# Kernel tuning notes

Measured on AMD Instinct MI355X. Metric: run time of the kernel, lower is better.

## Reference

```python
import jax, jax.numpy as jnp
import numpy as np

IN_SIZES = [64, 128, 256]
HIDDEN = [512, 512]
ENC = 256
COUNTS = [100000, 80000, 60000]


def _xavier(key, fan_in, fan_out):
    # xavier_uniform with gain('sigmoid') == 1
    lim = float(np.sqrt(6.0 / (fan_in + fan_out)))
    return jax.random.uniform(key, (fan_in, fan_out), jnp.float32, -lim, lim)


def setup_inputs() -> dict:
    key = jax.random.key(0)
    ks = jax.random.split(key, 32)
    inp = {}
    ki = 0
    for t, (n, d) in enumerate(zip(COUNTS, IN_SIZES)):
        inp[f"x{t}"] = jax.random.normal(ks[ki], (n, d), dtype=jnp.float32)
        ki += 1
    # node_type sorted by type, counts match x tensors (invariant of the module)
    inp["node_type"] = jnp.concatenate(
        [jnp.full((n,), t, dtype=jnp.int32) for t, n in enumerate(COUNTS)])
    for t, d_in in enumerate(IN_SIZES):
        sizes = [d_in] + HIDDEN + [ENC]
        for i in range(len(sizes) - 1):
            inp[f"W{t}_{i+1}"] = _xavier(ks[ki], sizes[i], sizes[i + 1])
            ki += 1
            inp[f"b{t}_{i+1}"] = jnp.zeros((sizes[i + 1],), jnp.float32)
    return inp


def _mlp(x, layers):
    # each layer is Linear followed by Sigmoid (including the last)
    for W, b in layers:
        x = jax.nn.sigmoid(x @ W + b)
    return x


def reference(x0, x1, x2, node_type,
              W0_1, b0_1, W0_2, b0_2, W0_3, b0_3,
              W1_1, b1_1, W1_2, b1_2, W1_3, b1_3,
              W2_1, b2_1, W2_2, b2_2, W2_3, b2_3):
    xs = [x0, x1, x2]
    params = [
        [(W0_1, b0_1), (W0_2, b0_2), (W0_3, b0_3)],
        [(W1_1, b1_1), (W1_2, b1_2), (W1_3, b1_3)],
        [(W2_1, b2_1), (W2_2, b2_2), (W2_3, b2_3)],
    ]
    N = node_type.shape[0]
    X = jnp.zeros((N, ENC), dtype=jnp.float32)
    for nt in range(len(xs)):
        # static per-type count -> fixed-size nonzero works under jit
        idx = jnp.nonzero(node_type == nt, size=xs[nt].shape[0])[0]
        X = X.at[idx].set(_mlp(xs[nt], params[nt]))
    return X
```

## Files before the change

kernel.cpp:

```cpp
#include <hip/hip_runtime.h>
#include <hip/hip_bf16.h>

typedef __bf16 bf16x8 __attribute__((ext_vector_type(8)));
typedef __bf16 bf16x4 __attribute__((ext_vector_type(4)));
typedef float  f32x16 __attribute__((ext_vector_type(16)));

#define BM 128
#define S  520
#define SF 260
#define NT 4

struct PrepParams {
    const float* src[9];
    int Kt[9];
    int Mg[9];
    int N[9];
    int blkEnd[9];
    int unitBase[9];
};

__global__ void __launch_bounds__(256)
prep_weights(PrepParams p, uint4* __restrict__ dst) {
    __shared__ float tile[32][128];
    int b = blockIdx.x;
    int w = 0;
    while (b >= p.blkEnd[w]) ++w;
    int local = b - ((w == 0) ? 0 : p.blkEnd[w - 1]);
    int mgc = p.Mg[w];
    int kt = local / mgc;
    int mg = local - kt * mgc;
    const float* src = p.src[w];
    int N = p.N[w];
    int Kc = p.Kt[w] * 2;
    int t = threadIdx.x;

    int row0 = kt * 32, col0 = mg * 128;
#pragma unroll
    for (int i = 0; i < 4; ++i) {
        int e4 = t + i * 256;
        int r = e4 >> 5;
        int c4 = e4 & 31;
        float4 v = *(const float4*)&src[(size_t)(row0 + r) * N + col0 + c4 * 4];
        *(float4*)&tile[r][c4 * 4] = v;
    }
    __syncthreads();

#pragma unroll
    for (int rep = 0; rep < 2; ++rep) {
        int ul = t + rep * 256;
        int lane = ul & 63;
        int kcl = (ul >> 6) & 1;
        int mtl = ul >> 7;
        int gUnit = p.unitBase[w] +
                    ((mg * 4 + mtl) * Kc + (kt * 2 + kcl)) * 64 + lane;
        int lr = kcl * 16 + ((lane >> 5) << 3);
        int lc = mtl * 32 + (lane & 31);
        alignas(16) unsigned short u8[8];
#pragma unroll
        for (int j = 0; j < 8; ++j)
            u8[j] = __builtin_bit_cast(unsigned short, (__bf16)tile[lr + j][lc]);
        dst[gUnit] = *(const uint4*)u8;
    }
}

struct MlpParams {
    const float* X[3];
    const unsigned short* Wp[3];
    const float* B1[3];
    const float* B2[3];
    const float* B3[3];
    int dIn[3];
    int Nt[3];
    int rowOff[3];
    int blkStart[3];
};

__device__ __forceinline__ float sigmoidf(float z) {
    return __builtin_amdgcn_rcpf(
        1.0f + __builtin_amdgcn_exp2f(-1.442695040888963f * z));
}

template <int KC, int MT, bool TO_LDS>
__device__ __forceinline__ void layer(
    unsigned short* __restrict__ buf,
    const unsigned short* __restrict__ W,
    const float* __restrict__ bias,
    int wave, int lane)
{
    const int half = lane >> 5;
    const int lr = lane & 31;

    f32x16 acc[NT][MT];
#pragma unroll
    for (int n = 0; n < NT; ++n)
#pragma unroll
        for (int m = 0; m < MT; ++m)
#pragma unroll
            for (int e = 0; e < 16; ++e)
                acc[n][m][e] = 0.0f;

    const unsigned short* bp = buf + lr * S + half * 8;
    const unsigned short* ap = W + (size_t)wave * MT * KC * 512 + lane * 8;

    bf16x8 aPf[4][MT];
#pragma unroll
    for (int p = 0; p < 4; ++p)
#pragma unroll
        for (int m = 0; m < MT; ++m)
            aPf[p][m] = *(const bf16x8*)(ap + ((size_t)m * KC + p) * 512);

#pragma unroll
    for (int kc = 0; kc < KC; ++kc) {
        bf16x8 b[NT];
#pragma unroll
        for (int n = 0; n < NT; ++n)
            b[n] = *(const bf16x8*)(bp + (size_t)n * 32 * S + kc * 16);
#pragma unroll
        for (int m = 0; m < MT; ++m)
#pragma unroll
            for (int n = 0; n < NT; ++n)
                acc[n][m] = __builtin_amdgcn_mfma_f32_32x32x16_bf16(
                    aPf[kc & 3][m], b[n], acc[n][m], 0, 0, 0);
        if (kc + 4 < KC) {
#pragma unroll
            for (int m = 0; m < MT; ++m)
                aPf[kc & 3][m] =
                    *(const bf16x8*)(ap + ((size_t)m * KC + (kc + 4)) * 512);
        }
    }

    __syncthreads();

#pragma unroll
    for (int m = 0; m < MT; ++m) {
        int mt = wave * MT + m;
#pragma unroll
        for (int g = 0; g < 4; ++g) {
            int f0 = mt * 32 + g * 8 + half * 4;
            float4 bv = *(const float4*)(bias + f0);
#pragma unroll
            for (int n = 0; n < NT; ++n) {
                int r = n * 32 + lr;
                float s0 = sigmoidf(acc[n][m][g * 4 + 0] + bv.x);
                float s1 = sigmoidf(acc[n][m][g * 4 + 1] + bv.y);
                float s2 = sigmoidf(acc[n][m][g * 4 + 2] + bv.z);
                float s3 = sigmoidf(acc[n][m][g * 4 + 3] + bv.w);
                if constexpr (TO_LDS) {
                    bf16x4 h = {(__bf16)s0, (__bf16)s1, (__bf16)s2, (__bf16)s3};
                    *(bf16x4*)(buf + r * S + f0) = h;
                } else {
                    float* fb = (float*)buf;
                    *(float4*)(fb + r * SF + f0) =
                        make_float4(s0, s1, s2, s3);
                }
            }
        }
    }
}

__global__ void __launch_bounds__(512, 2)
mlp_fused(MlpParams p, float* __restrict__ out) {
    extern __shared__ unsigned short buf[];

    int nwg = gridDim.x;
    int bid = blockIdx.x;
    int q = nwg >> 3, r8 = nwg & 7;
    int xcd = bid & 7, lid = bid >> 3;
    int b = (xcd < r8 ? xcd * (q + 1) : r8 * (q + 1) + (xcd - r8) * q) + lid;

    int t = (b >= p.blkStart[1]) + (b >= p.blkStart[2]);
    int blk = b - p.blkStart[t];
    int dIn = p.dIn[t];
    int Nt = p.Nt[t];
    int row0 = blk * BM;
    const float* X = p.X[t];
    const unsigned short* W1 = p.Wp[t];
    const unsigned short* W2 = W1 + dIn * 512;
    const unsigned short* W3 = W2 + 512 * 512;

    int tid = threadIdx.x;
    int wave = tid >> 6;
    int lane = tid & 63;

    int d4 = dIn >> 2;
    int s4 = 31 - __clz(d4);
    int nf4 = BM * d4;
    for (int i = tid; i < nf4; i += 512) {
        int r = i >> s4;
        int c4 = i & (d4 - 1);
        int grow = row0 + r;
        float4 v = make_float4(0.f, 0.f, 0.f, 0.f);
        if (grow < Nt) v = ((const float4*)X)[(size_t)grow * d4 + c4];
        ushort4 u;
        u.x = __builtin_bit_cast(unsigned short, (__bf16)v.x);
        u.y = __builtin_bit_cast(unsigned short, (__bf16)v.y);
        u.z = __builtin_bit_cast(unsigned short, (__bf16)v.z);
        u.w = __builtin_bit_cast(unsigned short, (__bf16)v.w);
        *(ushort4*)(buf + r * S + c4 * 4) = u;
    }
    __syncthreads();

    if (t == 0)      layer< 4, 2, true>(buf, W1, p.B1[t], wave, lane);
    else if (t == 1) layer< 8, 2, true>(buf, W1, p.B1[t], wave, lane);
    else             layer<16, 2, true>(buf, W1, p.B1[t], wave, lane);
    __syncthreads();
    layer<32, 2, true>(buf, W2, p.B2[t], wave, lane);
    __syncthreads();
    layer<32, 1, false>(buf, W3, p.B3[t], wave, lane);
    __syncthreads();

    const float* fb = (const float*)buf;
    float* gOut = out + (size_t)(p.rowOff[t] + row0) * 256;
    for (int i = tid; i < BM * 64; i += 512) {
        int r = i >> 6;
        int c4 = i & 63;
        if (row0 + r < Nt)
            *(float4*)(gOut + r * 256 + c4 * 4) =
                *(const float4*)(fb + r * SF + c4 * 4);
    }
}

extern "C" void kernel_launch(void* const* d_in, const int* in_sizes, int n_in,
                              void* d_out, int out_size, void* d_ws, size_t ws_size,
                              hipStream_t stream) {
    const int IN0[3] = {64, 128, 256};
    const int CNT[3] = {100000, 80000, 60000};

    PrepParams pp;
    int blocks = 0, ubase = 0;
    for (int t = 0; t < 3; ++t) {
        int Ks[3] = {IN0[t], 512, 512};
        int Ns[3] = {512, 512, 256};
        for (int l = 0; l < 3; ++l) {
            int w = t * 3 + l;
            pp.src[w] = (const float*)d_in[4 + t * 6 + l * 2];
            pp.Kt[w] = Ks[l] >> 5;
            pp.Mg[w] = Ns[l] >> 7;
            pp.N[w] = Ns[l];
            pp.unitBase[w] = ubase;
            blocks += pp.Kt[w] * pp.Mg[w];
            pp.blkEnd[w] = blocks;
            ubase += (Ks[l] * Ns[l]) >> 3;
        }
    }
    prep_weights<<<dim3(blocks), dim3(256), 0, stream>>>(pp, (uint4*)d_ws);

    MlpParams mp;
    int woff = 0, roff = 0, boff = 0;
    for (int t = 0; t < 3; ++t) {
        mp.X[t] = (const float*)d_in[t];
        mp.Wp[t] = (const unsigned short*)d_ws + woff;
        mp.B1[t] = (const float*)d_in[4 + t * 6 + 1];
        mp.B2[t] = (const float*)d_in[4 + t * 6 + 3];
        mp.B3[t] = (const float*)d_in[4 + t * 6 + 5];
        mp.dIn[t] = IN0[t];
        mp.Nt[t] = CNT[t];
        mp.rowOff[t] = roff;
        mp.blkStart[t] = boff;
        woff += IN0[t] * 512 + 512 * 512 + 512 * 256;
        roff += CNT[t];
        boff += (CNT[t] + BM - 1) / BM;
    }
    size_t lds = (size_t)BM * S * sizeof(unsigned short);
    mlp_fused<<<dim3(boff), dim3(512), lds, stream>>>(mp, (float*)d_out);
}
```

Before: 657.9 us.

## Stream weights into LDS ring via async global-to-LDS loads with swizzled activations

Restructures the fused MLP kernel so each workgroup handles 64 rows with 4 waves. Weight tiles are no longer loaded per wave from global into registers; they are streamed into a double-buffered LDS ring with global_load_lds and consumed under explicit barriers and wait counts. The activation buffer uses an XOR swizzle in place of row padding, and the prepped weight layout is reordered to suit the new streaming order. This trades fewer rows per block, which means more weight traffic per output row, plus two barriers per k-step, for weight reuse shared across waves and loads that overlap the MFMAs.

```diff
diff --git a/kernel.cpp b/kernel.cpp
--- a/kernel.cpp
+++ b/kernel.cpp
@@ -5,10 +5,8 @@
 typedef __bf16 bf16x4 __attribute__((ext_vector_type(4)));
 typedef float  f32x16 __attribute__((ext_vector_type(16)));
 
-#define BM 128
-#define S  520
-#define SF 260
-#define NT 4
+#define MFMA __builtin_amdgcn_mfma_f32_32x32x16_bf16
+#define BM 64
 
 struct PrepParams {
     const float* src[9];
@@ -31,7 +29,6 @@
     int mg = local - kt * mgc;
     const float* src = p.src[w];
     int N = p.N[w];
-    int Kc = p.Kt[w] * 2;
     int t = threadIdx.x;
 
     int row0 = kt * 32, col0 = mg * 128;
@@ -51,8 +48,11 @@
         int lane = ul & 63;
         int kcl = (ul >> 6) & 1;
         int mtl = ul >> 7;
-        int gUnit = p.unitBase[w] +
-                    ((mg * 4 + mtl) * Kc + (kt * 2 + kcl)) * 64 + lane;
+        int mt = mg * 4 + mtl;
+        int k16 = kt * 2 + kcl;
+        int pidx = (N == 512) ? (k16 * 2 + (mt >> 3)) : k16;
+        int ml = mt & 7;
+        int gUnit = p.unitBase[w] + (pidx * 8 + ml) * 64 + lane;
         int lr = kcl * 16 + ((lane >> 5) << 3);
         int lc = mtl * 32 + (lane & 31);
         alignas(16) unsigned short u8[8];
@@ -80,87 +80,148 @@
         1.0f + __builtin_amdgcn_exp2f(-1.442695040888963f * z));
 }
 
-template <int KC, int MT, bool TO_LDS>
-__device__ __forceinline__ void layer(
-    unsigned short* __restrict__ buf,
-    const unsigned short* __restrict__ W,
-    const float* __restrict__ bias,
-    int wave, int lane)
+__device__ __forceinline__ unsigned swz(unsigned o) {
+    return o ^ (((o >> 10) & 31) << 4);
+}
+
+__device__ __forceinline__ void gload_lds16(const void* g, void* l) {
+    __builtin_amdgcn_global_load_lds(
+        (const __attribute__((address_space(1))) unsigned int*)g,
+        (__attribute__((address_space(3))) unsigned int*)l, 16, 0, 0);
+}
+
+__device__ __forceinline__ void halfstep(
+    const char* act, unsigned bo0, unsigned bo1, int k16,
+    const unsigned short* rc, unsigned short* rn,
+    const uint4*& wsrc, bool pf, int wave, int lane,
+    f32x16& a00, f32x16& a01, f32x16& a10, f32x16& a11)
 {
-    const int half = lane >> 5;
-    const int lr = lane & 31;
-
-    f32x16 acc[NT][MT];
-#pragma unroll
-    for (int n = 0; n < NT; ++n)
-#pragma unroll
-        for (int m = 0; m < MT; ++m)
-#pragma unroll
-            for (int e = 0; e < 16; ++e)
-                acc[n][m][e] = 0.0f;
-
-    const unsigned short* bp = buf + lr * S + half * 8;
-    const unsigned short* ap = W + (size_t)wave * MT * KC * 512 + lane * 8;
-
-    bf16x8 aPf[4][MT];
-#pragma unroll
-    for (int p = 0; p < 4; ++p)
-#pragma unroll
-        for (int m = 0; m < MT; ++m)
-            aPf[p][m] = *(const bf16x8*)(ap + ((size_t)m * KC + p) * 512);
-
-#pragma unroll
-    for (int kc = 0; kc < KC; ++kc) {
-        bf16x8 b[NT];
-#pragma unroll
-        for (int n = 0; n < NT; ++n)
-            b[n] = *(const bf16x8*)(bp + (size_t)n * 32 * S + kc * 16);
-#pragma unroll
-        for (int m = 0; m < MT; ++m)
-#pragma unroll
-            for (int n = 0; n < NT; ++n)
-                acc[n][m] = __builtin_amdgcn_mfma_f32_32x32x16_bf16(
-                    aPf[kc & 3][m], b[n], acc[n][m], 0, 0, 0);
-        if (kc + 4 < KC) {
-#pragma unroll
-            for (int m = 0; m < MT; ++m)
-                aPf[kc & 3][m] =
-                    *(const bf16x8*)(ap + ((size_t)m * KC + (kc + 4)) * 512);
+    unsigned o0 = bo0 + (unsigned)k16 * 32;
+    unsigned o1 = bo1 + (unsigned)k16 * 32;
+    bf16x8 b0 = *(const bf16x8*)(act + swz(o0));
+    bf16x8 b1 = *(const bf16x8*)(act + swz(o1));
+    if (pf) {
+        gload_lds16(wsrc + wave * 128 + lane,      rn + wave * 1024);
+        gload_lds16(wsrc + wave * 128 + 64 + lane, rn + wave * 1024 + 512);
+        wsrc += 512;
+        asm volatile("s_waitcnt vmcnt(2)" ::: "memory");
+    } else {
+        asm volatile("s_waitcnt vmcnt(0)" ::: "memory");
+    }
+    asm volatile("s_barrier" ::: "memory");
+    const unsigned short* ap = rc + wave * 1024 + lane * 8;
+    bf16x8 va0 = *(const bf16x8*)ap;
+    bf16x8 va1 = *(const bf16x8*)(ap + 512);
+    __builtin_amdgcn_s_setprio(1);
+    a00 = MFMA(va0, b0, a00, 0, 0, 0);
+    a10 = MFMA(va0, b1, a10, 0, 0, 0);
+    a01 = MFMA(va1, b0, a01, 0, 0, 0);
+    a11 = MFMA(va1, b1, a11, 0, 0, 0);
+    __builtin_amdgcn_s_setprio(0);
+    asm volatile("s_barrier" ::: "memory");
+}
+
+template <int K16>
+__device__ __forceinline__ void layer512(
+    char* act, unsigned short* ring, const uint4*& wsrc,
+    const float* bias, int wave, int lane, unsigned bo0, unsigned bo1)
+{
+    f32x16 acc[2][2][2];
+#pragma unroll
+    for (int h = 0; h < 2; ++h)
+#pragma unroll
+      for (int b = 0; b < 2; ++b)
+#pragma unroll
+        for (int m = 0; m < 2; ++m)
+#pragma unroll
+          for (int e = 0; e < 16; ++e) acc[h][b][m][e] = 0.f;
+
+#pragma unroll 2
+    for (int k16 = 0; k16 < K16; ++k16) {
+        halfstep(act, bo0, bo1, k16, ring,        ring + 4096, wsrc, true, wave, lane,
+                 acc[0][0][0], acc[0][0][1], acc[0][1][0], acc[0][1][1]);
+        halfstep(act, bo0, bo1, k16, ring + 4096, ring,        wsrc, true, wave, lane,
+                 acc[1][0][0], acc[1][0][1], acc[1][1][0], acc[1][1][1]);
+    }
+
+    int hv = lane >> 5, lr = lane & 31;
+#pragma unroll
+    for (int h = 0; h < 2; ++h)
+#pragma unroll
+      for (int m = 0; m < 2; ++m) {
+        int mt = h * 8 + wave * 2 + m;
+#pragma unroll
+        for (int g = 0; g < 4; ++g) {
+          int f0 = mt * 32 + g * 8 + hv * 4;
+          float4 bv = *(const float4*)(bias + f0);
+#pragma unroll
+          for (int bt = 0; bt < 2; ++bt) {
+            int r = bt * 32 + lr;
+            float s0 = sigmoidf(acc[h][bt][m][g * 4 + 0] + bv.x);
+            float s1 = sigmoidf(acc[h][bt][m][g * 4 + 1] + bv.y);
+            float s2 = sigmoidf(acc[h][bt][m][g * 4 + 2] + bv.z);
+            float s3 = sigmoidf(acc[h][bt][m][g * 4 + 3] + bv.w);
+            bf16x4 h4 = {(__bf16)s0, (__bf16)s1, (__bf16)s2, (__bf16)s3};
+            unsigned o = (unsigned)r * 1024 + (unsigned)f0 * 2;
+            *(bf16x4*)(act + swz(o)) = h4;
+          }
         }
-    }
-
-    __syncthreads();
-
-#pragma unroll
-    for (int m = 0; m < MT; ++m) {
-        int mt = wave * MT + m;
+      }
+    asm volatile("s_waitcnt lgkmcnt(0)" ::: "memory");
+    asm volatile("s_barrier" ::: "memory");
+}
+
+template <int K16>
+__device__ __forceinline__ void layer256(
+    char* act, unsigned short* ring, const uint4*& wsrc,
+    const float* bias, int wave, int lane, unsigned bo0, unsigned bo1)
+{
+    f32x16 acc[2][2];
+#pragma unroll
+    for (int b = 0; b < 2; ++b)
+#pragma unroll
+      for (int m = 0; m < 2; ++m)
+#pragma unroll
+        for (int e = 0; e < 16; ++e) acc[b][m][e] = 0.f;
+
+#pragma unroll 2
+    for (int kp = 0; kp < K16; kp += 2) {
+        halfstep(act, bo0, bo1, kp,     ring,        ring + 4096, wsrc, true,
+                 wave, lane, acc[0][0], acc[0][1], acc[1][0], acc[1][1]);
+        halfstep(act, bo0, bo1, kp + 1, ring + 4096, ring,        wsrc, (kp + 2 < K16),
+                 wave, lane, acc[0][0], acc[0][1], acc[1][0], acc[1][1]);
+    }
+
+    int hv = lane >> 5, lr = lane & 31;
+#pragma unroll
+    for (int m = 0; m < 2; ++m) {
+        int mt = wave * 2 + m;
 #pragma unroll
         for (int g = 0; g < 4; ++g) {
-            int f0 = mt * 32 + g * 8 + half * 4;
+            int f0 = mt * 32 + g * 8 + hv * 4;
             float4 bv = *(const float4*)(bias + f0);
 #pragma unroll
-            for (int n = 0; n < NT; ++n) {
-                int r = n * 32 + lr;
-                float s0 = sigmoidf(acc[n][m][g * 4 + 0] + bv.x);
-                float s1 = sigmoidf(acc[n][m][g * 4 + 1] + bv.y);
-                float s2 = sigmoidf(acc[n][m][g * 4 + 2] + bv.z);
-                float s3 = sigmoidf(acc[n][m][g * 4 + 3] + bv.w);
-                if constexpr (TO_LDS) {
-                    bf16x4 h = {(__bf16)s0, (__bf16)s1, (__bf16)s2, (__bf16)s3};
-                    *(bf16x4*)(buf + r * S + f0) = h;
-                } else {
-                    float* fb = (float*)buf;
-                    *(float4*)(fb + r * SF + f0) =
-                        make_float4(s0, s1, s2, s3);
-                }
+            for (int bt = 0; bt < 2; ++bt) {
+                int r = bt * 32 + lr;
+                float4 o4;
+                o4.x = sigmoidf(acc[bt][m][g * 4 + 0] + bv.x);
+                o4.y = sigmoidf(acc[bt][m][g * 4 + 1] + bv.y);
+                o4.z = sigmoidf(acc[bt][m][g * 4 + 2] + bv.z);
+                o4.w = sigmoidf(acc[bt][m][g * 4 + 3] + bv.w);
+                unsigned o = (unsigned)r * 1024 + (unsigned)f0 * 4;
+                *(float4*)(act + swz(o)) = o4;
             }
         }
     }
-}
-
-__global__ void __launch_bounds__(512, 2)
+    asm volatile("s_waitcnt lgkmcnt(0)" ::: "memory");
+    asm volatile("s_barrier" ::: "memory");
+}
+
+__global__ void __launch_bounds__(256, 2)
 mlp_fused(MlpParams p, float* __restrict__ out) {
-    extern __shared__ unsigned short buf[];
+    extern __shared__ char smem[];
+    char* act = smem;
+    unsigned short* ring = (unsigned short*)(smem + 65536);
 
     int nwg = gridDim.x;
     int bid = blockIdx.x;
@@ -174,18 +235,20 @@
     int Nt = p.Nt[t];
     int row0 = blk * BM;
     const float* X = p.X[t];
-    const unsigned short* W1 = p.Wp[t];
-    const unsigned short* W2 = W1 + dIn * 512;
-    const unsigned short* W3 = W2 + 512 * 512;
+    const uint4* wsrc = (const uint4*)p.Wp[t];
 
     int tid = threadIdx.x;
     int wave = tid >> 6;
     int lane = tid & 63;
 
+    gload_lds16(wsrc + wave * 128 + lane,      ring + wave * 1024);
+    gload_lds16(wsrc + wave * 128 + 64 + lane, ring + wave * 1024 + 512);
+    wsrc += 512;
+
     int d4 = dIn >> 2;
     int s4 = 31 - __clz(d4);
     int nf4 = BM * d4;
-    for (int i = tid; i < nf4; i += 512) {
+    for (int i = tid; i < nf4; i += 256) {
         int r = i >> s4;
         int c4 = i & (d4 - 1);
         int grow = row0 + r;
@@ -196,27 +259,28 @@
         u.y = __builtin_bit_cast(unsigned short, (__bf16)v.y);
         u.z = __builtin_bit_cast(unsigned short, (__bf16)v.z);
         u.w = __builtin_bit_cast(unsigned short, (__bf16)v.w);
-        *(ushort4*)(buf + r * S + c4 * 4) = u;
+        unsigned o = (unsigned)r * 1024 + (unsigned)c4 * 8;
+        *(ushort4*)(act + swz(o)) = u;
     }
     __syncthreads();
 
-    if (t == 0)      layer< 4, 2, true>(buf, W1, p.B1[t], wave, lane);
-    else if (t == 1) layer< 8, 2, true>(buf, W1, p.B1[t], wave, lane);
-    else             layer<16, 2, true>(buf, W1, p.B1[t], wave, lane);
-    __syncthreads();
-    layer<32, 2, true>(buf, W2, p.B2[t], wave, lane);
-    __syncthreads();
-    layer<32, 1, false>(buf, W3, p.B3[t], wave, lane);
-    __syncthreads();
-
-    const float* fb = (const float*)buf;
+    unsigned bo0 = (unsigned)(lane & 31) * 1024 + (unsigned)(lane >> 5) * 16;
+    unsigned bo1 = bo0 + 32 * 1024;
+
+    if (t == 0)      layer512<4 >(act, ring, wsrc, p.B1[0], wave, lane, bo0, bo1);
+    else if (t == 1) layer512<8 >(act, ring, wsrc, p.B1[1], wave, lane, bo0, bo1);
+    else             layer512<16>(act, ring, wsrc, p.B1[2], wave, lane, bo0, bo1);
+    layer512<32>(act, ring, wsrc, p.B2[t], wave, lane, bo0, bo1);
+    layer256<32>(act, ring, wsrc, p.B3[t], wave, lane, bo0, bo1);
+
     float* gOut = out + (size_t)(p.rowOff[t] + row0) * 256;
-    for (int i = tid; i < BM * 64; i += 512) {
+    for (int i = tid; i < BM * 64; i += 256) {
         int r = i >> 6;
         int c4 = i & 63;
-        if (row0 + r < Nt)
-            *(float4*)(gOut + r * 256 + c4 * 4) =
-                *(const float4*)(fb + r * SF + c4 * 4);
+        if (row0 + r < Nt) {
+            unsigned o = (unsigned)r * 1024 + (unsigned)c4 * 16;
+            *(float4*)(gOut + r * 256 + c4 * 4) = *(const float4*)(act + swz(o));
+        }
     }
 }
 
@@ -261,6 +325,6 @@
         roff += CNT[t];
         boff += (CNT[t] + BM - 1) / BM;
     }
-    size_t lds = (size_t)BM * S * sizeof(unsigned short);
-    mlp_fused<<<dim3(boff), dim3(512), lds, stream>>>(mp, (float*)d_out);
-}
+    size_t lds = 65536 + 2 * 8192;
+    mlp_fused<<<dim3(boff), dim3(256), lds, stream>>>(mp, (float*)d_out);
+}
```

New measurement: 707.8 us. 1.08x slower.

## Replace padded LDS activation layout with XOR swizzle and k-major weight packing

Applied to the files above, without the earlier changes.

The activation buffer changes from padded rows (stride 520 halves) to a dense 1024-byte row layout with an XOR swizzle, which cuts LDS use from about 133KB to 128KB and is meant to avoid bank conflicts. Packed weights are reordered k-major, so all m-tiles for one k-step sit next to each other, and the prefetch loop is restructured around that order. Barriers move inside the layer function. The risk is that the swizzle does not remove conflicts for the 16-byte B reads as well as padding did, and the different global access pattern for weights.

```diff
diff --git a/kernel.cpp b/kernel.cpp
--- a/kernel.cpp
+++ b/kernel.cpp
@@ -5,10 +5,8 @@
 typedef __bf16 bf16x4 __attribute__((ext_vector_type(4)));
 typedef float  f32x16 __attribute__((ext_vector_type(16)));
 
+#define MFMA __builtin_amdgcn_mfma_f32_32x32x16_bf16
 #define BM 128
-#define S  520
-#define SF 260
-#define NT 4
 
 struct PrepParams {
     const float* src[9];
@@ -31,7 +29,7 @@
     int mg = local - kt * mgc;
     const float* src = p.src[w];
     int N = p.N[w];
-    int Kc = p.Kt[w] * 2;
+    int NU = N >> 5;
     int t = threadIdx.x;
 
     int row0 = kt * 32, col0 = mg * 128;
@@ -51,8 +49,9 @@
         int lane = ul & 63;
         int kcl = (ul >> 6) & 1;
         int mtl = ul >> 7;
-        int gUnit = p.unitBase[w] +
-                    ((mg * 4 + mtl) * Kc + (kt * 2 + kcl)) * 64 + lane;
+        int mt = mg * 4 + mtl;
+        int k16 = kt * 2 + kcl;
+        int gUnit = p.unitBase[w] + (k16 * NU + mt) * 64 + lane;
         int lr = kcl * 16 + ((lane >> 5) << 3);
         int lc = mtl * 32 + (lane & 31);
         alignas(16) unsigned short u8[8];
@@ -80,53 +79,61 @@
         1.0f + __builtin_amdgcn_exp2f(-1.442695040888963f * z));
 }
 
-template <int KC, int MT, bool TO_LDS>
-__device__ __forceinline__ void layer(
-    unsigned short* __restrict__ buf,
-    const unsigned short* __restrict__ W,
+__device__ __forceinline__ unsigned swz(unsigned o) {
+    return o ^ (((o >> 10) & 31) << 4);
+}
+
+template <int K16, int NU, int MT, bool TO_LDS>
+__device__ __forceinline__ void layerR(
+    char* __restrict__ act,
+    const uint4* __restrict__ W,
     const float* __restrict__ bias,
     int wave, int lane)
 {
+    const int lr = lane & 31;
     const int half = lane >> 5;
-    const int lr = lane & 31;
-
-    f32x16 acc[NT][MT];
-#pragma unroll
-    for (int n = 0; n < NT; ++n)
+    const unsigned xm = (unsigned)lr << 4;
+    const unsigned bo = (unsigned)lr * 1024u + (unsigned)half * 16u;
+
+    f32x16 acc[MT][4];
+#pragma unroll
+    for (int m = 0; m < MT; ++m)
+#pragma unroll
+        for (int bt = 0; bt < 4; ++bt)
+#pragma unroll
+            for (int e = 0; e < 16; ++e) acc[m][bt][e] = 0.f;
+
+    const uint4* ap = W + (size_t)(wave * MT) * 64 + lane;
+
+    bf16x8 aPf[4][MT];
+#pragma unroll
+    for (int d = 0; d < 4; ++d)
 #pragma unroll
         for (int m = 0; m < MT; ++m)
-#pragma unroll
-            for (int e = 0; e < 16; ++e)
-                acc[n][m][e] = 0.0f;
-
-    const unsigned short* bp = buf + lr * S + half * 8;
-    const unsigned short* ap = W + (size_t)wave * MT * KC * 512 + lane * 8;
-
-    bf16x8 aPf[4][MT];
-#pragma unroll
-    for (int p = 0; p < 4; ++p)
+            aPf[d][m] = *(const bf16x8*)(ap + (size_t)(d * NU + m) * 64);
+
+#pragma unroll
+    for (int k = 0; k < K16; ++k) {
+        bf16x8 b[4];
+#pragma unroll
+        for (int bt = 0; bt < 4; ++bt) {
+            unsigned o = bo + (unsigned)bt * 32768u + (unsigned)k * 32u;
+            b[bt] = *(const bf16x8*)(act + (o ^ xm));
+        }
+        bf16x8 av[MT];
+#pragma unroll
+        for (int m = 0; m < MT; ++m) av[m] = aPf[k & 3][m];
+        if (k + 4 < K16) {
+#pragma unroll
+            for (int m = 0; m < MT; ++m)
+                aPf[k & 3][m] =
+                    *(const bf16x8*)(ap + (size_t)((k + 4) * NU + m) * 64);
+        }
 #pragma unroll
         for (int m = 0; m < MT; ++m)
-            aPf[p][m] = *(const bf16x8*)(ap + ((size_t)m * KC + p) * 512);
-
-#pragma unroll
-    for (int kc = 0; kc < KC; ++kc) {
-        bf16x8 b[NT];
-#pragma unroll
-        for (int n = 0; n < NT; ++n)
-            b[n] = *(const bf16x8*)(bp + (size_t)n * 32 * S + kc * 16);
-#pragma unroll
-        for (int m = 0; m < MT; ++m)
-#pragma unroll
-            for (int n = 0; n < NT; ++n)
-                acc[n][m] = __builtin_amdgcn_mfma_f32_32x32x16_bf16(
-                    aPf[kc & 3][m], b[n], acc[n][m], 0, 0, 0);
-        if (kc + 4 < KC) {
-#pragma unroll
-            for (int m = 0; m < MT; ++m)
-                aPf[kc & 3][m] =
-                    *(const bf16x8*)(ap + ((size_t)m * KC + (kc + 4)) * 512);
-        }
+#pragma unroll
+            for (int bt = 0; bt < 4; ++bt)
+                acc[m][bt] = MFMA(av[m], b[bt], acc[m][bt], 0, 0, 0);
     }
 
     __syncthreads();
@@ -139,28 +146,28 @@
             int f0 = mt * 32 + g * 8 + half * 4;
             float4 bv = *(const float4*)(bias + f0);
 #pragma unroll
-            for (int n = 0; n < NT; ++n) {
-                int r = n * 32 + lr;
-                float s0 = sigmoidf(acc[n][m][g * 4 + 0] + bv.x);
-                float s1 = sigmoidf(acc[n][m][g * 4 + 1] + bv.y);
-                float s2 = sigmoidf(acc[n][m][g * 4 + 2] + bv.z);
-                float s3 = sigmoidf(acc[n][m][g * 4 + 3] + bv.w);
+            for (int bt = 0; bt < 4; ++bt) {
+                int r = bt * 32 + lr;
+                float s0 = sigmoidf(acc[m][bt][g * 4 + 0] + bv.x);
+                float s1 = sigmoidf(acc[m][bt][g * 4 + 1] + bv.y);
+                float s2 = sigmoidf(acc[m][bt][g * 4 + 2] + bv.z);
+                float s3 = sigmoidf(acc[m][bt][g * 4 + 3] + bv.w);
                 if constexpr (TO_LDS) {
-                    bf16x4 h = {(__bf16)s0, (__bf16)s1, (__bf16)s2, (__bf16)s3};
-                    *(bf16x4*)(buf + r * S + f0) = h;
+                    bf16x4 h4 = {(__bf16)s0, (__bf16)s1, (__bf16)s2, (__bf16)s3};
+                    *(bf16x4*)(act + swz((unsigned)r * 1024u + (unsigned)f0 * 2u)) = h4;
                 } else {
-                    float* fb = (float*)buf;
-                    *(float4*)(fb + r * SF + f0) =
+                    *(float4*)(act + swz((unsigned)r * 1024u + (unsigned)f0 * 4u)) =
                         make_float4(s0, s1, s2, s3);
                 }
             }
         }
     }
+    __syncthreads();
 }
 
 __global__ void __launch_bounds__(512, 2)
 mlp_fused(MlpParams p, float* __restrict__ out) {
-    extern __shared__ unsigned short buf[];
+    extern __shared__ char act[];
 
     int nwg = gridDim.x;
     int bid = blockIdx.x;
@@ -174,9 +181,9 @@
     int Nt = p.Nt[t];
     int row0 = blk * BM;
     const float* X = p.X[t];
-    const unsigned short* W1 = p.Wp[t];
-    const unsigned short* W2 = W1 + dIn * 512;
-    const unsigned short* W3 = W2 + 512 * 512;
+    const uint4* W1u = (const uint4*)p.Wp[t];
+    const uint4* W2u = W1u + ((size_t)dIn * 512 >> 3);
+    const uint4* W3u = W2u + ((size_t)512 * 512 >> 3);
 
     int tid = threadIdx.x;
     int wave = tid >> 6;
@@ -196,27 +203,25 @@
         u.y = __builtin_bit_cast(unsigned short, (__bf16)v.y);
         u.z = __builtin_bit_cast(unsigned short, (__bf16)v.z);
         u.w = __builtin_bit_cast(unsigned short, (__bf16)v.w);
-        *(ushort4*)(buf + r * S + c4 * 4) = u;
-    }
-    __syncthreads();
-
-    if (t == 0)      layer< 4, 2, true>(buf, W1, p.B1[t], wave, lane);
-    else if (t == 1) layer< 8, 2, true>(buf, W1, p.B1[t], wave, lane);
-    else             layer<16, 2, true>(buf, W1, p.B1[t], wave, lane);
-    __syncthreads();
-    layer<32, 2, true>(buf, W2, p.B2[t], wave, lane);
-    __syncthreads();
-    layer<32, 1, false>(buf, W3, p.B3[t], wave, lane);
-    __syncthreads();
-
-    const float* fb = (const float*)buf;
+        unsigned o = (unsigned)r * 1024u + (unsigned)c4 * 8u;
+        *(ushort4*)(act + swz(o)) = u;
+    }
+    __syncthreads();
+
+    if (t == 0)      layerR<4,  16, 2, true >(act, W1u, p.B1[0], wave, lane);
+    else if (t == 1) layerR<8,  16, 2, true >(act, W1u, p.B1[1], wave, lane);
+    else             layerR<16, 16, 2, true >(act, W1u, p.B1[2], wave, lane);
+    layerR<32, 16, 2, true >(act, W2u, p.B2[t], wave, lane);
+    layerR<32,  8, 1, false>(act, W3u, p.B3[t], wave, lane);
+
     float* gOut = out + (size_t)(p.rowOff[t] + row0) * 256;
     for (int i = tid; i < BM * 64; i += 512) {
         int r = i >> 6;
         int c4 = i & 63;
-        if (row0 + r < Nt)
-            *(float4*)(gOut + r * 256 + c4 * 4) =
-                *(const float4*)(fb + r * SF + c4 * 4);
+        if (row0 + r < Nt) {
+            unsigned o = (unsigned)r * 1024u + (unsigned)c4 * 16u;
+            *(float4*)(gOut + r * 256 + c4 * 4) = *(const float4*)(act + swz(o));
+        }
     }
 }
 
@@ -261,6 +266,6 @@
         roff += CNT[t];
         boff += (CNT[t] + BM - 1) / BM;
     }
-    size_t lds = (size_t)BM * S * sizeof(unsigned short);
+    size_t lds = (size_t)BM * 1024;
     mlp_fused<<<dim3(boff), dim3(512), lds, stream>>>(mp, (float*)d_out);
 }
```

New measurement: 926.8 us. 1.41x slower.
